# Performance work log

Measured on AMD Instinct MI355X. Metric: run time of the kernel, lower is better.

## Reference

```python
import jax, jax.numpy as jnp
import numpy as np

N, E, IN, HID, HEADS, OUT = 20000, 320000, 128, 64, 8, 64
NEG_SLOPE = 0.2  # PyG GATConv default leaky_relu slope


def setup_inputs() -> dict:
    key = jax.random.key(0)
    ks = jax.random.split(key, 12)
    g = lambda k, shape, fan_in: jax.random.normal(k, shape, jnp.float32) / np.sqrt(fan_in)
    return {
        "x": jax.random.normal(ks[0], (N, IN), jnp.float32),
        "edge_index": jax.random.randint(ks[1], (2, E), 0, N, jnp.int32),
        "W1": g(ks[2], (IN, HEADS * HID), IN),
        "att_src1": g(ks[3], (HEADS, HID), HID),
        "att_dst1": g(ks[4], (HEADS, HID), HID),
        "b1": jnp.zeros((HEADS * HID,), jnp.float32),
        "W2": g(ks[5], (HEADS * HID, OUT), HEADS * HID),
        "att_src2": g(ks[6], (1, OUT), OUT),
        "att_dst2": g(ks[7], (1, OUT), OUT),
        "b2": jnp.zeros((OUT,), jnp.float32),
    }


def gat_conv(x, edge_index, W, att_src, att_dst, b, heads, out_ch):
    """PyG-style GATConv with add_self_loops=True, concat=True."""
    n = x.shape[0]
    loop = jnp.arange(n, dtype=edge_index.dtype)
    src = jnp.concatenate([edge_index[0], loop])  # message source nodes
    dst = jnp.concatenate([edge_index[1], loop])  # aggregation targets

    h = (x @ W).reshape(n, heads, out_ch)               # [N,H,C]
    a_s = jnp.sum(h * att_src[None], axis=-1)            # [N,H]
    a_d = jnp.sum(h * att_dst[None], axis=-1)            # [N,H]

    e = jax.nn.leaky_relu(a_s[src] + a_d[dst], NEG_SLOPE)  # [Etot,H]
    # numerically stable edge-softmax over incoming neighborhoods
    m = jax.ops.segment_max(e, dst, num_segments=n)
    m = jnp.where(jnp.isfinite(m), m, 0.0)
    p = jnp.exp(e - m[dst])
    denom = jax.ops.segment_sum(p, dst, num_segments=n)
    alpha = p / denom[dst]                               # [Etot,H]

    out = jax.ops.segment_sum(h[src] * alpha[:, :, None], dst, num_segments=n)  # [N,H,C]
    return out.reshape(n, heads * out_ch) + b


def reference(x, edge_index, W1, att_src1, att_dst1, b1, W2, att_src2, att_dst2, b2):
    h = gat_conv(x, edge_index, W1, att_src1, att_dst1, b1, HEADS, HID)
    h = jax.nn.relu(h)
    out = gat_conv(h, edge_index, W2, att_src2, att_dst2, b2, 1, OUT)
    return out
```

## Files before the change

kernel.cpp:

```cpp
#include <hip/hip_runtime.h>
#include <cstdint>

#define N_NODES 20000
#define N_EDGES 320000
#define ET (N_EDGES + N_NODES)
#define IN_DIM 128
#define HID 64
#define HEADS 8
#define F1 (HEADS * HID)
#define OUT_DIM 64
#define NEG_SLOPE 0.2f
#define NB_SCAN 20

typedef __attribute__((ext_vector_type(8))) short bf16x8;
typedef __attribute__((ext_vector_type(4))) float f32x4;

__device__ __forceinline__ ushort f2bf(float f) {
  uint32_t u = __float_as_uint(f);
  uint32_t r = (u + 0x7fffu + ((u >> 16) & 1u)) >> 16;
  return (ushort)r;
}
__device__ __forceinline__ float bfu_lo(uint32_t p) { return __uint_as_float(p << 16); }
__device__ __forceinline__ float bfu_hi(uint32_t p) { return __uint_as_float(p & 0xffff0000u); }
__device__ __forceinline__ float lrelu(float x) { return x > 0.f ? x : NEG_SLOPE * x; }

__global__ void prep_kernel(const float* __restrict__ x, const float* __restrict__ W1,
                            const float* __restrict__ W2, ushort* __restrict__ xb,
                            ushort* __restrict__ W1T, ushort* __restrict__ W2T,
                            int* __restrict__ deg) {
  const int NX4 = N_NODES * IN_DIM / 4;
  const int E1 = NX4 + IN_DIM * F1;
  const int E2 = E1 + F1 * OUT_DIM;
  int idx = blockIdx.x * 256 + threadIdx.x;
  if (idx < NX4) {
    float4 v = reinterpret_cast<const float4*>(x)[idx];
    ushort4 o;
    o.x = f2bf(v.x); o.y = f2bf(v.y); o.z = f2bf(v.z); o.w = f2bf(v.w);
    reinterpret_cast<ushort4*>(xb)[idx] = o;
  } else if (idx < E1) {
    int k = idx - NX4;
    int r = k / F1, c = k - r * F1;
    W1T[(size_t)c * IN_DIM + r] = f2bf(W1[k]);
  } else if (idx < E2) {
    int k = idx - E1;
    int r = k / OUT_DIM, c = k - r * OUT_DIM;
    W2T[(size_t)c * F1 + r] = f2bf(W2[k]);
  } else if (idx < E2 + N_NODES) {
    deg[idx - E2] = 0;
  }
}

__global__ void hist_kernel(const int* __restrict__ ei, int* __restrict__ deg) {
  int e = blockIdx.x * 256 + threadIdx.x;
  if (e >= ET) return;
  int dst = (e < N_EDGES) ? ei[N_EDGES + e] : (e - N_EDGES);
  atomicAdd(&deg[dst], 1);
}

__global__ __launch_bounds__(1024) void scan_a(const int* __restrict__ deg,
                                               int* __restrict__ off,
                                               int* __restrict__ bsum) {
  __shared__ int wsum[16];
  int i = blockIdx.x * 1024 + threadIdx.x;
  int lane = threadIdx.x & 63, wid = threadIdx.x >> 6;
  int v = (i < N_NODES) ? deg[i] : 0;
  int s = v;
#pragma unroll
  for (int d = 1; d < 64; d <<= 1) {
    int u = __shfl_up(s, d);
    if (lane >= d) s += u;
  }
  if (lane == 63) wsum[wid] = s;
  __syncthreads();
  if (wid == 0) {
    int ws = (lane < 16) ? wsum[lane] : 0;
#pragma unroll
    for (int d = 1; d < 16; d <<= 1) {
      int u = __shfl_up(ws, d);
      if (lane >= d) ws += u;
    }
    if (lane < 16) wsum[lane] = ws;
  }
  __syncthreads();
  int wbase = (wid > 0) ? wsum[wid - 1] : 0;
  int incl = wbase + s;
  if (i < N_NODES) off[i] = incl - v;
  if (threadIdx.x == 1023) bsum[blockIdx.x] = incl;
}

__global__ __launch_bounds__(1024) void scan_c(const int* __restrict__ bsum,
                                               int* __restrict__ off,
                                               int* __restrict__ pos) {
  int b = blockIdx.x;
  int pre = 0, tot = 0;
#pragma unroll
  for (int k = 0; k < NB_SCAN; ++k) {
    int v = bsum[k];
    if (k < b) pre += v;
    tot += v;
  }
  int i = b * 1024 + threadIdx.x;
  if (i < N_NODES) {
    int o = off[i] + pre;
    off[i] = o;
    pos[i] = o;
  }
  if (b == 0 && threadIdx.x == 0) off[N_NODES] = tot;
}

__global__ void scatter_kernel(const int* __restrict__ ei, int* __restrict__ pos,
                               int* __restrict__ csr_src) {
  int e = blockIdx.x * 256 + threadIdx.x;
  if (e >= ET) return;
  int src, dst;
  if (e < N_EDGES) { src = ei[e]; dst = ei[N_EDGES + e]; }
  else             { src = e - N_EDGES; dst = src; }
  int slot = atomicAdd(&pos[dst], 1);
  csr_src[slot] = src;
}

__device__ __forceinline__ int swz(int r, int kg) { return kg ^ ((r >> 1) & 3); }

template <int WR, int WC, int TM, int TN, int ASD>
__global__ __launch_bounds__(256) void gemm_kernel(
    const ushort* __restrict__ A, const ushort* __restrict__ BT,
    ushort* __restrict__ Cb, int M, int K, int NC,
    const float* __restrict__ atts, const float* __restrict__ attd,
    float* __restrict__ asd) {
  constexpr int BM = WR * TM * 16;
  constexpr int BN = WC * TN * 16;
  __shared__ ushort As[BM * 32];
  __shared__ ushort Bs[BN * 32];
  const int t = threadIdx.x;
  const int lane = t & 63, wid = t >> 6;
  const int wr = wid / WC, wc = wid % WC;
  const int m0 = blockIdx.y * BM, n0 = blockIdx.x * BN;
  f32x4 acc[TM][TN] = {};
  const int srow = t >> 2, kg = t & 3;

  for (int k0 = 0; k0 < K; k0 += 32) {
#pragma unroll
    for (int q = 0; q < BM / 64; ++q) {
      int r = srow + 64 * q;
      int gr = m0 + r; if (gr >= M) gr = M - 1;
      bf16x8 v = *reinterpret_cast<const bf16x8*>(&A[(size_t)gr * K + k0 + kg * 8]);
      *reinterpret_cast<bf16x8*>(&As[r * 32 + swz(r, kg) * 8]) = v;
    }
#pragma unroll
    for (int q = 0; q < BN / 64; ++q) {
      int r = srow + 64 * q;
      int gn = n0 + r;
      bf16x8 v = *reinterpret_cast<const bf16x8*>(&BT[(size_t)gn * K + k0 + kg * 8]);
      *reinterpret_cast<bf16x8*>(&Bs[r * 32 + swz(r, kg) * 8]) = v;
    }
    __syncthreads();
    int kq = lane >> 4;
    int rr = lane & 15;
    bf16x8 af[TM], bfv[TN];
#pragma unroll
    for (int i = 0; i < TM; ++i) {
      int r = (wr * TM + i) * 16 + rr;
      af[i] = *reinterpret_cast<const bf16x8*>(&As[r * 32 + swz(r, kq) * 8]);
    }
#pragma unroll
    for (int j = 0; j < TN; ++j) {
      int r = (wc * TN + j) * 16 + rr;
      bfv[j] = *reinterpret_cast<const bf16x8*>(&Bs[r * 32 + swz(r, kq) * 8]);
    }
#pragma unroll
    for (int i = 0; i < TM; ++i)
#pragma unroll
      for (int j = 0; j < TN; ++j)
        acc[i][j] = __builtin_amdgcn_mfma_f32_16x16x32_bf16(af[i], bfv[j], acc[i][j], 0, 0, 0);
    __syncthreads();
  }
  const int cr0 = (lane >> 4) * 4;
  const int cc = lane & 15;
#pragma unroll
  for (int i = 0; i < TM; ++i)
#pragma unroll
    for (int j = 0; j < TN; ++j)
#pragma unroll
      for (int r = 0; r < 4; ++r) {
        int gm = m0 + (wr * TM + i) * 16 + cr0 + r;
        int gn = n0 + (wc * TN + j) * 16 + cc;
        if (gm < M) Cb[(size_t)gm * NC + gn] = f2bf(acc[i][j][r]);
      }
  if constexpr (ASD != 0) {
    static_assert(TN * 16 == 64, "asd fusion needs 64-col wave tile");
    const int hh = (ASD == 1) ? ((n0 + wc * 64) >> 6) : 0;
    float as_v[TN], ad_v[TN];
#pragma unroll
    for (int j = 0; j < TN; ++j) {
      as_v[j] = atts[hh * 64 + j * 16 + cc];
      ad_v[j] = attd[hh * 64 + j * 16 + cc];
    }
#pragma unroll
    for (int i = 0; i < TM; ++i)
#pragma unroll
      for (int r = 0; r < 4; ++r) {
        float ps = 0.f, pd = 0.f;
#pragma unroll
        for (int j = 0; j < TN; ++j) {
          ps += acc[i][j][r] * as_v[j];
          pd += acc[i][j][r] * ad_v[j];
        }
#pragma unroll
        for (int s = 1; s < 16; s <<= 1) {
          ps += __shfl_xor(ps, s);
          pd += __shfl_xor(pd, s);
        }
        int row = m0 + (wr * TM + i) * 16 + cr0 + r;
        if (cc == 0 && row < M) {
          if constexpr (ASD == 1) {
            asd[(size_t)row * 16 + hh] = ps;
            asd[(size_t)row * 16 + 8 + hh] = pd;
          } else {
            asd[(size_t)row * 2 + 0] = ps;
            asd[(size_t)row * 2 + 1] = pd;
          }
        }
      }
  }
}

__global__ __launch_bounds__(64) void agg1_kernel(
    const int* __restrict__ off, const int* __restrict__ csrs,
    const float* __restrict__ asd, const ushort* __restrict__ H1b,
    const float* __restrict__ b1, ushort* __restrict__ X2b) {
  __shared__ float w_lds[64];
  __shared__ int src_lds[16];
  int bid = blockIdx.x;
  int x = bid & 7;
  int phase = x >> 2;
  int node = (bid >> 3) * 4 + (x & 3);
  int lane = threadIdx.x;
  int hl = lane >> 4, j = lane & 15;
  int head = phase * 4 + hl;
  int s0 = off[node], s1 = off[node + 1];
  float adst = asd[(size_t)node * 16 + 8 + head];
  const uint2* Hp = reinterpret_cast<const uint2*>(H1b);
  const int uoff = head * 16 + j;
  float s = 0.f;
  float a0 = 0.f, a1 = 0.f, a2 = 0.f, a3 = 0.f;
  for (int c0 = s0; c0 < s1; c0 += 16) {
    int n = s1 - c0; if (n > 16) n = 16;
    int src = (j < n) ? csrs[c0 + j] : 0;
    if (lane < 16) src_lds[lane] = src;
    float wv = (j < n) ? __expf(lrelu(asd[(size_t)src * 16 + head] + adst)) : 0.f;
    w_lds[lane] = wv;
    int i = 0;
    for (; i + 2 <= n; i += 2) {
      int sA = src_lds[i], sB = src_lds[i + 1];
      float wA = w_lds[hl * 16 + i], wB = w_lds[hl * 16 + i + 1];
      uint2 pA = Hp[(size_t)sA * 128 + uoff];
      uint2 pB = Hp[(size_t)sB * 128 + uoff];
      s += wA + wB;
      a0 += wA * bfu_lo(pA.x) + wB * bfu_lo(pB.x);
      a1 += wA * bfu_hi(pA.x) + wB * bfu_hi(pB.x);
      a2 += wA * bfu_lo(pA.y) + wB * bfu_lo(pB.y);
      a3 += wA * bfu_hi(pA.y) + wB * bfu_hi(pB.y);
    }
    if (i < n) {
      int sA = src_lds[i];
      float wA = w_lds[hl * 16 + i];
      uint2 p = Hp[(size_t)sA * 128 + uoff];
      s += wA;
      a0 += wA * bfu_lo(p.x); a1 += wA * bfu_hi(p.x);
      a2 += wA * bfu_lo(p.y); a3 += wA * bfu_hi(p.y);
    }
  }
  float inv = 1.f / s;
  int fb = head * 64 + j * 4;
  float v0 = fmaxf(a0 * inv + b1[fb], 0.f);
  float v1 = fmaxf(a1 * inv + b1[fb + 1], 0.f);
  float v2 = fmaxf(a2 * inv + b1[fb + 2], 0.f);
  float v3 = fmaxf(a3 * inv + b1[fb + 3], 0.f);
  uint2 o;
  o.x = (uint32_t)f2bf(v0) | ((uint32_t)f2bf(v1) << 16);
  o.y = (uint32_t)f2bf(v2) | ((uint32_t)f2bf(v3) << 16);
  reinterpret_cast<uint2*>(X2b)[(size_t)node * 128 + uoff] = o;
}

__global__ __launch_bounds__(256) void agg2_kernel(
    const int* __restrict__ off, const int* __restrict__ csrs,
    const float* __restrict__ asd, const ushort* __restrict__ H2b,
    const float* __restrict__ b2, float* __restrict__ out) {
  __shared__ float w_lds[4][64];
  __shared__ int src_lds[4][64];
  int wv_id = threadIdx.x >> 6;
  int node = blockIdx.x * 4 + wv_id;
  if (node >= N_NODES) return;
  int lane = threadIdx.x & 63;
  int grp = lane >> 4, fr = lane & 15;
  int s0 = off[node], s1 = off[node + 1];
  float adst = asd[(size_t)node * 2 + 1];
  const uint2* Hp = reinterpret_cast<const uint2*>(H2b);
  float s = 0.f;
  float a0 = 0.f, a1 = 0.f, a2 = 0.f, a3 = 0.f;
  for (int c0 = s0; c0 < s1; c0 += 64) {
    int n = s1 - c0; if (n > 64) n = 64;
    int src = (lane < n) ? csrs[c0 + lane] : 0;
    float wv = (lane < n) ? __expf(lrelu(asd[(size_t)src * 2] + adst)) : 0.f;
    src_lds[wv_id][lane] = src;
    w_lds[wv_id][lane] = wv;
    int i = grp;
    for (; i + 4 < n; i += 8) {
      int sA = src_lds[wv_id][i], sB = src_lds[wv_id][i + 4];
      float wA = w_lds[wv_id][i], wB = w_lds[wv_id][i + 4];
      uint2 pA = Hp[(size_t)sA * 16 + fr];
      uint2 pB = Hp[(size_t)sB * 16 + fr];
      s += wA + wB;
      a0 += wA * bfu_lo(pA.x) + wB * bfu_lo(pB.x);
      a1 += wA * bfu_hi(pA.x) + wB * bfu_hi(pB.x);
      a2 += wA * bfu_lo(pA.y) + wB * bfu_lo(pB.y);
      a3 += wA * bfu_hi(pA.y) + wB * bfu_hi(pB.y);
    }
    if (i < n) {
      int sA = src_lds[wv_id][i];
      float wA = w_lds[wv_id][i];
      uint2 p = Hp[(size_t)sA * 16 + fr];
      s += wA;
      a0 += wA * bfu_lo(p.x); a1 += wA * bfu_hi(p.x);
      a2 += wA * bfu_lo(p.y); a3 += wA * bfu_hi(p.y);
    }
  }
#pragma unroll
  for (int d = 16; d < 64; d <<= 1) {
    a0 += __shfl_xor(a0, d);
    a1 += __shfl_xor(a1, d);
    a2 += __shfl_xor(a2, d);
    a3 += __shfl_xor(a3, d);
    s  += __shfl_xor(s, d);
  }
  if (grp == 0) {
    float inv = 1.f / s;
    int fb = fr * 4;
    float4 o;
    o.x = a0 * inv + b2[fb];
    o.y = a1 * inv + b2[fb + 1];
    o.z = a2 * inv + b2[fb + 2];
    o.w = a3 * inv + b2[fb + 3];
    reinterpret_cast<float4*>(out)[(size_t)node * 16 + fr] = o;
  }
}

extern "C" void kernel_launch(void* const* d_in, const int* in_sizes, int n_in,
                              void* d_out, int out_size, void* d_ws, size_t ws_size,
                              hipStream_t stream) {
  const float* x        = (const float*)d_in[0];
  const int*   ei       = (const int*)  d_in[1];
  const float* W1       = (const float*)d_in[2];
  const float* att_src1 = (const float*)d_in[3];
  const float* att_dst1 = (const float*)d_in[4];
  const float* b1       = (const float*)d_in[5];
  const float* W2       = (const float*)d_in[6];
  const float* att_src2 = (const float*)d_in[7];
  const float* att_dst2 = (const float*)d_in[8];
  const float* b2       = (const float*)d_in[9];
  float* out = (float*)d_out;

  char* w = (char*)d_ws;
  auto alloc = [&](size_t bytes) {
    char* p = w;
    w += (bytes + 255) & ~(size_t)255;
    return p;
  };
  ushort* xb     = (ushort*)alloc((size_t)N_NODES * IN_DIM * 2);
  ushort* W1T    = (ushort*)alloc((size_t)F1 * IN_DIM * 2);
  ushort* W2T    = (ushort*)alloc((size_t)OUT_DIM * F1 * 2);
  ushort* H1b    = (ushort*)alloc((size_t)N_NODES * F1 * 2);
  ushort* X2b    = (ushort*)alloc((size_t)N_NODES * F1 * 2);
  ushort* H2b    = (ushort*)alloc((size_t)N_NODES * OUT_DIM * 2);
  float* asd1    = (float*)alloc((size_t)N_NODES * 16 * 4);
  float* asd2    = (float*)alloc((size_t)N_NODES * 2 * 4);
  int* deg       = (int*)alloc((size_t)N_NODES * 4);
  int* off       = (int*)alloc((size_t)(N_NODES + 1) * 4);
  int* pos       = (int*)alloc((size_t)N_NODES * 4);
  int* csrsrc    = (int*)alloc((size_t)ET * 4);
  int* bsum      = (int*)alloc((size_t)NB_SCAN * 4);

  {
    int total = N_NODES * IN_DIM / 4 + IN_DIM * F1 + F1 * OUT_DIM + N_NODES;
    prep_kernel<<<(total + 255) / 256, 256, 0, stream>>>(x, W1, W2, xb, W1T, W2T, deg);
  }

  hist_kernel<<<(ET + 255) / 256, 256, 0, stream>>>(ei, deg);
  scan_a<<<NB_SCAN, 1024, 0, stream>>>(deg, off, bsum);
  scan_c<<<NB_SCAN, 1024, 0, stream>>>(bsum, off, pos);
  scatter_kernel<<<(ET + 255) / 256, 256, 0, stream>>>(ei, pos, csrsrc);

  gemm_kernel<2, 2, 4, 4, 1>
      <<<dim3(F1 / 128, (N_NODES + 127) / 128), 256, 0, stream>>>(
      xb, W1T, H1b, N_NODES, IN_DIM, F1, att_src1, att_dst1, asd1);
  agg1_kernel<<<2 * N_NODES, 64, 0, stream>>>(off, csrsrc, asd1, H1b, b1, X2b);

  gemm_kernel<4, 1, 1, 4, 2>
      <<<dim3(1, (N_NODES + 63) / 64), 256, 0, stream>>>(
      X2b, W2T, H2b, N_NODES, F1, OUT_DIM, att_src2, att_dst2, asd2);
  agg2_kernel<<<(N_NODES + 3) / 4, 256, 0, stream>>>(off, csrsrc, asd2, H2b, b2, out);
}
```

Measured before the change: 136.4 us.

## Restructure layer-1 aggregation to one head per wave with edge-split groups

Layer-1 aggregation is remapped so that each 256-thread block handles four nodes for a single head, one wave per node. The wave's four 16-lane groups split the incoming edges (stride 4) and combine their partial sums with cross-lane shuffles before writing. Previously a 64-thread block covered four heads of one node, with each group walking every edge serially. The aim is more memory-level parallelism per edge chain and fewer short serial loops on high-degree nodes. The cost is shuffle reductions, three idle groups at write-out, and each 16-edge chunk's source and weight values being recomputed once per head.

```diff
diff --git a/kernel.cpp b/kernel.cpp
--- a/kernel.cpp
+++ b/kernel.cpp
@@ -224,37 +224,34 @@
   }
 }
 
-__global__ __launch_bounds__(64) void agg1_kernel(
+__global__ __launch_bounds__(256) void agg1_kernel(
     const int* __restrict__ off, const int* __restrict__ csrs,
     const float* __restrict__ asd, const ushort* __restrict__ H1b,
     const float* __restrict__ b1, ushort* __restrict__ X2b) {
-  __shared__ float w_lds[64];
-  __shared__ int src_lds[16];
+  __shared__ float w_lds[4][16];
+  __shared__ int src_lds[4][16];
   int bid = blockIdx.x;
-  int x = bid & 7;
-  int phase = x >> 2;
-  int node = (bid >> 3) * 4 + (x & 3);
-  int lane = threadIdx.x;
-  int hl = lane >> 4, j = lane & 15;
-  int head = phase * 4 + hl;
+  int head = bid & 7;
+  int wv = threadIdx.x >> 6;
+  int node = (bid >> 3) * 4 + wv;
+  int lane = threadIdx.x & 63;
+  int grp = lane >> 4, fr = lane & 15;
   int s0 = off[node], s1 = off[node + 1];
   float adst = asd[(size_t)node * 16 + 8 + head];
-  const uint2* Hp = reinterpret_cast<const uint2*>(H1b);
-  const int uoff = head * 16 + j;
+  const uint2* Hh = reinterpret_cast<const uint2*>(H1b) + head * 16;
   float s = 0.f;
   float a0 = 0.f, a1 = 0.f, a2 = 0.f, a3 = 0.f;
   for (int c0 = s0; c0 < s1; c0 += 16) {
     int n = s1 - c0; if (n > 16) n = 16;
-    int src = (j < n) ? csrs[c0 + j] : 0;
-    if (lane < 16) src_lds[lane] = src;
-    float wv = (j < n) ? __expf(lrelu(asd[(size_t)src * 16 + head] + adst)) : 0.f;
-    w_lds[lane] = wv;
-    int i = 0;
-    for (; i + 2 <= n; i += 2) {
-      int sA = src_lds[i], sB = src_lds[i + 1];
-      float wA = w_lds[hl * 16 + i], wB = w_lds[hl * 16 + i + 1];
-      uint2 pA = Hp[(size_t)sA * 128 + uoff];
-      uint2 pB = Hp[(size_t)sB * 128 + uoff];
+    int src = (fr < n) ? csrs[c0 + fr] : 0;
+    float wv_ = (fr < n) ? __expf(lrelu(asd[(size_t)src * 16 + head] + adst)) : 0.f;
+    if (grp == 0) { src_lds[wv][fr] = src; w_lds[wv][fr] = wv_; }
+    int i = grp;
+    for (; i + 4 < n; i += 8) {
+      int sA = src_lds[wv][i], sB = src_lds[wv][i + 4];
+      float wA = w_lds[wv][i], wB = w_lds[wv][i + 4];
+      uint2 pA = Hh[(size_t)sA * 128 + fr];
+      uint2 pB = Hh[(size_t)sB * 128 + fr];
       s += wA + wB;
       a0 += wA * bfu_lo(pA.x) + wB * bfu_lo(pB.x);
       a1 += wA * bfu_hi(pA.x) + wB * bfu_hi(pB.x);
@@ -262,24 +259,34 @@
       a3 += wA * bfu_hi(pA.y) + wB * bfu_hi(pB.y);
     }
     if (i < n) {
-      int sA = src_lds[i];
-      float wA = w_lds[hl * 16 + i];
-      uint2 p = Hp[(size_t)sA * 128 + uoff];
+      int sA = src_lds[wv][i];
+      float wA = w_lds[wv][i];
+      uint2 p = Hh[(size_t)sA * 128 + fr];
       s += wA;
       a0 += wA * bfu_lo(p.x); a1 += wA * bfu_hi(p.x);
       a2 += wA * bfu_lo(p.y); a3 += wA * bfu_hi(p.y);
     }
   }
-  float inv = 1.f / s;
-  int fb = head * 64 + j * 4;
-  float v0 = fmaxf(a0 * inv + b1[fb], 0.f);
-  float v1 = fmaxf(a1 * inv + b1[fb + 1], 0.f);
-  float v2 = fmaxf(a2 * inv + b1[fb + 2], 0.f);
-  float v3 = fmaxf(a3 * inv + b1[fb + 3], 0.f);
-  uint2 o;
-  o.x = (uint32_t)f2bf(v0) | ((uint32_t)f2bf(v1) << 16);
-  o.y = (uint32_t)f2bf(v2) | ((uint32_t)f2bf(v3) << 16);
-  reinterpret_cast<uint2*>(X2b)[(size_t)node * 128 + uoff] = o;
+#pragma unroll
+  for (int d = 16; d < 64; d <<= 1) {
+    a0 += __shfl_xor(a0, d);
+    a1 += __shfl_xor(a1, d);
+    a2 += __shfl_xor(a2, d);
+    a3 += __shfl_xor(a3, d);
+    s  += __shfl_xor(s, d);
+  }
+  if (grp == 0) {
+    float inv = 1.f / s;
+    int fb = head * 64 + fr * 4;
+    float v0 = fmaxf(a0 * inv + b1[fb], 0.f);
+    float v1 = fmaxf(a1 * inv + b1[fb + 1], 0.f);
+    float v2 = fmaxf(a2 * inv + b1[fb + 2], 0.f);
+    float v3 = fmaxf(a3 * inv + b1[fb + 3], 0.f);
+    uint2 o;
+    o.x = (uint32_t)f2bf(v0) | ((uint32_t)f2bf(v1) << 16);
+    o.y = (uint32_t)f2bf(v2) | ((uint32_t)f2bf(v3) << 16);
+    reinterpret_cast<uint2*>(X2b)[(size_t)node * 128 + head * 16 + fr] = o;
+  }
 }
 
 __global__ __launch_bounds__(256) void agg2_kernel(
@@ -393,7 +400,7 @@
   gemm_kernel<2, 2, 4, 4, 1>
       <<<dim3(F1 / 128, (N_NODES + 127) / 128), 256, 0, stream>>>(
       xb, W1T, H1b, N_NODES, IN_DIM, F1, att_src1, att_dst1, asd1);
-  agg1_kernel<<<2 * N_NODES, 64, 0, stream>>>(off, csrsrc, asd1, H1b, b1, X2b);
+  agg1_kernel<<<HEADS * (N_NODES / 4), 256, 0, stream>>>(off, csrsrc, asd1, H1b, b1, X2b);
 
   gemm_kernel<4, 1, 1, 4, 2>
       <<<dim3(1, (N_NODES + 63) / 64), 256, 0, stream>>>(
```

Result: slower. 166.8 us (+22.3%).
